# Kernel tuning notes

Hardware: AMD Instinct MI355X
Metric: run time of the kernel (lower is better)

Reference implementation:

```python
import jax, jax.numpy as jnp
import numpy as np
from jax import lax

EPS = 1e-8

def setup_inputs() -> dict:
    key = jax.random.key(0)
    ks = jax.random.split(key, 9)
    B, Cin, H, W = 16, 128, 64, 64
    C = 256
    return {
        "x":  jax.random.normal(ks[0], (B, Cin, H, W), jnp.float32),
        "w1": jax.random.normal(ks[1], (C, Cin, 3, 3), jnp.float32) * 0.02,
        "b1": jax.random.normal(ks[2], (C,), jnp.float32) * 0.02,
        "w2": jax.random.normal(ks[3], (C, C), jnp.float32) * 0.02,
        "b2": jax.random.normal(ks[4], (C,), jnp.float32) * 0.02,
        "w3": jax.random.normal(ks[5], (C, C), jnp.float32) * 0.02,
        "b3": jax.random.normal(ks[6], (C,), jnp.float32) * 0.02,
        "w4": jax.random.normal(ks[7], (C, C), jnp.float32) * 0.02,
        "b4": jax.random.normal(ks[8], (C,), jnp.float32) * 0.02,
    }

def reference(x, w1, b1, w2, b2, w3, b3, w4, b4):
    B = x.shape[0]
    # conv1: 3x3, pad 1 -> [B, 256, H, W]
    conv1 = lax.conv_general_dilated(
        x, w1, window_strides=(1, 1), padding="SAME",
        dimension_numbers=("NCHW", "OIHW", "NCHW")) + b1[None, :, None, None]
    H, W = conv1.shape[2], conv1.shape[3]
    C = conv1.shape[1]
    # gap1 -> [B, 256]; note: forward never applies relu/sigmoid (faithful)
    gap1 = conv1.mean(axis=(2, 3))
    c2 = gap1 @ w2.T + b2            # 1x1 conv on 1x1 spatial == dense
    c3 = c2 @ w3.T + b3              # [B, 256]
    # add1 = conv1 + conv1 * c3 (broadcast scale over spatial)
    add1 = conv1 * (1.0 + c3[:, :, None, None])
    gap2 = add1.mean(axis=(2, 3))    # [B, 256]
    # cosine similarity along channel dim between gap2 and add1 -> [B, H, W]
    num = jnp.einsum("bc,bchw->bhw", gap2, add1)
    n_g = jnp.maximum(jnp.linalg.norm(gap2, axis=1), EPS)[:, None, None]
    n_a = jnp.maximum(jnp.sqrt(jnp.sum(add1 * add1, axis=1)), EPS)
    cos = num / (n_g * n_a)
    r1 = cos.reshape(B, H * W)       # [B, HW]
    m1 = r1.T @ r1                   # [HW, HW] cross-batch position similarity
    # conv4: 1x1 conv -> [B, 256, H, W]
    conv4 = jnp.einsum("oc,bchw->bohw", w4, add1) + b4[None, :, None, None]
    # torch: permute to NHWC then view as [B, 256, HW] (mixes dims; faithful)
    r2 = jnp.transpose(conv4, (0, 2, 3, 1)).reshape(B, C, H * W)
    m2 = r2 @ m1                     # [B, 256, HW]
    return m2.reshape(B, C, H, W)
```

## Files before the change

kernel.cpp:

```cpp
#include <hip/hip_runtime.h>

#define EPSF 1e-8f

typedef __attribute__((ext_vector_type(8))) short bf16x8;
typedef __attribute__((ext_vector_type(16))) float f32x16;

#define MFMA32(a, b, c) __builtin_amdgcn_mfma_f32_32x32x16_bf16(a, b, c, 0, 0, 0)

__device__ __forceinline__ uint32_t splitpack(float v) {
    uint32_t u = __float_as_uint(v);
    uint32_t hb = (u + 0x7fffu + ((u >> 16) & 1u)) & 0xffff0000u;
    float rem = v - __uint_as_float(hb);
    uint32_t r = __float_as_uint(rem);
    uint32_t lb = (r + 0x7fffu + ((r >> 16) & 1u)) >> 16;
    return (hb >> 16) | (lb << 16);
}
__device__ __forceinline__ float unpackf(uint32_t p) {
    return __uint_as_float(p << 16) + __uint_as_float(p & 0xffff0000u);
}

__device__ __forceinline__ void gload_lds16(const void* src, void* dst) {
#if __has_builtin(__builtin_amdgcn_global_load_lds)
    __builtin_amdgcn_global_load_lds(
        (const __attribute__((address_space(1))) uint32_t*)src,
        (__attribute__((address_space(3))) uint32_t*)dst, 16, 0, 0);
#else
    *(uint4*)dst = *(const uint4*)src;
#endif
}

__global__ __launch_bounds__(256) void k_xpack(const float* __restrict__ x,
                                               unsigned short* __restrict__ xph,
                                               unsigned short* __restrict__ xpl) {
    const int bx = blockIdx.x;
    const int hb = bx & 15, cg = (bx >> 4) & 15, b = bx >> 8;
    const int tid = threadIdx.x;
    const int w = tid & 63, hs = tid >> 6;
    const int h = hb * 4 + hs;
    uint32_t hiw[4], low[4];
#pragma unroll
    for (int q = 0; q < 4; ++q) {
        uint32_t u0 = splitpack(x[(((b * 128 + cg * 8 + q * 2) * 64) + h) * 64 + w]);
        uint32_t u1 = splitpack(x[(((b * 128 + cg * 8 + q * 2 + 1) * 64) + h) * 64 + w]);
        hiw[q] = (u0 & 0xffffu) | (u1 << 16);
        low[q] = (u0 >> 16) | (u1 & 0xffff0000u);
    }
    const long o = ((((long)(b * 16 + cg) * 64 + h) * 64) + w) * 8;
    *(uint4*)(xph + o) = *(uint4*)hiw;
    *(uint4*)(xpl + o) = *(uint4*)low;
}

__global__ __launch_bounds__(256) void k_wpack(const float* __restrict__ w1,
                                               short* __restrict__ Bh, short* __restrict__ Bl) {
    int d = blockIdx.x * 256 + threadIdx.x;
    int j = d & 7, lane = (d >> 3) & 63, nt = (d >> 9) & 7, cp = (d >> 12) & 7, tap = d >> 15;
    int oc = nt * 32 + (lane & 31);
    int cin = cp * 16 + (lane >> 5) * 8 + j;
    uint32_t u = splitpack(w1[oc * 1152 + cin * 9 + tap]);
    Bh[d] = (short)(u & 0xffffu);
    Bl[d] = (short)(u >> 16);
}

__global__ __launch_bounds__(512, 2) void k_conv1(
        const unsigned short* __restrict__ xph, const unsigned short* __restrict__ xpl,
        const short* __restrict__ Bh, const short* __restrict__ Bl,
        const float* __restrict__ b1,
        uint32_t* __restrict__ c1p, float* __restrict__ gpart) {
    __shared__ uint4 lds[2 * 2 * 12 * 66];
    const int bxr = blockIdx.x;
    const int bx = ((bxr & 7) << 6) | (bxr >> 3);
    const int ot = bx & 1, hp = (bx >> 1) & 15, b = bx >> 5;
    const int h0 = hp * 4;
    const int tid = threadIdx.x;
    const int lane = tid & 63, wv = tid >> 6;
    const int mq = wv >> 1, nh = wv & 1;
    const int l31 = lane & 31, hbit = lane >> 5;

    f32x16 acc[2][2];
#pragma unroll
    for (int i = 0; i < 2; ++i)
#pragma unroll
        for (int j = 0; j < 2; ++j)
#pragma unroll
            for (int r = 0; r < 16; ++r) acc[i][j][r] = 0.f;

    auto stage = [&](int buf, int cp) {
#pragma unroll
        for (int i = 0; i < 3; ++i) {
            const int id = wv * 3 + i;
            const int plane = (id >= 12) ? 1 : 0;
            const int u = id - plane * 12;
            const int r6 = u >> 1, kg = u & 1;
            const int grow = h0 - 1 + r6;
            uint4* dst = &lds[((buf * 2 + plane) * 12 + u) * 66 + 1 + lane];
            if ((unsigned)grow < 64u) {
                const unsigned short* pls = plane ? xpl : xph;
                const unsigned short* src =
                    pls + ((((long)(b * 16 + cp * 2 + kg) * 64 + grow) * 64) + lane) * 8;
                gload_lds16(src, dst);
            } else {
                *dst = (uint4){0u, 0u, 0u, 0u};
            }
        }
    };

    stage(0, 0);
    if (tid < 96) {
        const int row = tid >> 1, side = tid & 1;
        lds[row * 66 + (side ? 65 : 0)] = (uint4){0u, 0u, 0u, 0u};
    }
    __syncthreads();

    bf16x8 Ahv[2][2], Alv[2][2], Bhv[3][2], Blv[3][2];
#define LOADA(tap_, par) do {                                                     \
        const int kh_ = (tap_) / 3, kw_ = (tap_) % 3;                             \
        _Pragma("unroll")                                                         \
        for (int mt = 0; mt < 2; ++mt) {                                          \
            const int rb = ((buf * 2 + 0) * 12 + (mq + kh_) * 2 + hbit) * 66      \
                           + kw_ + mt * 32 + l31;                                 \
            Ahv[par][mt] = *(const bf16x8*)&lds[rb];                              \
            Alv[par][mt] = *(const bf16x8*)&lds[rb + 12 * 66];                    \
        } } while (0)
#define LOADB(cp_, tap_, par) do {                                                \
        _Pragma("unroll")                                                         \
        for (int nt = 0; nt < 2; ++nt) {                                          \
            const int fi = (((tap_) * 8 + (cp_)) * 8 + ot * 4 + nh * 2 + nt) * 512 + lane * 8; \
            Bhv[par][nt] = *(const bf16x8*)(Bh + fi);                             \
            Blv[par][nt] = *(const bf16x8*)(Bl + fi);                             \
        } } while (0)

    LOADB(0, 0, 0);
    LOADB(0, 1, 1);
    int buf = 0;
    for (int cp = 0; cp < 8; ++cp) {
        if (cp < 7) stage(buf ^ 1, cp + 1);
        LOADA(0, 0);
#pragma unroll
        for (int tap = 0; tap < 9; ++tap) {
            if (tap < 7) {
                LOADB(cp, tap + 2, (tap + 2) % 3);
            } else if (cp < 7) {
                LOADB(cp + 1, tap - 7, (tap + 2) % 3);
            }
            if (tap < 8) LOADA(tap + 1, (tap + 1) & 1);
            const int ab = tap & 1, bb = tap % 3;
            __builtin_amdgcn_s_setprio(1);
#pragma unroll
            for (int nt = 0; nt < 2; ++nt)
#pragma unroll
                for (int mt = 0; mt < 2; ++mt) {
                    acc[mt][nt] = MFMA32(Ahv[ab][mt], Bhv[bb][nt], acc[mt][nt]);
                    acc[mt][nt] = MFMA32(Ahv[ab][mt], Blv[bb][nt], acc[mt][nt]);
                    acc[mt][nt] = MFMA32(Alv[ab][mt], Bhv[bb][nt], acc[mt][nt]);
                }
            __builtin_amdgcn_s_setprio(0);
        }
        __syncthreads();
        buf ^= 1;
    }
#undef LOADA
#undef LOADB

    const int hrow = h0 + mq;
#pragma unroll
    for (int nt = 0; nt < 2; ++nt) {
        const int oc = ot * 128 + (nh * 2 + nt) * 32 + l31;
        float g = 0.f;
#pragma unroll
        for (int mt = 0; mt < 2; ++mt)
#pragma unroll
            for (int r = 0; r < 16; ++r) g += acc[mt][nt][r];
        g += __shfl_xor(g, 32);
        if (hbit == 0) gpart[((b * 16 + hp) * 4 + mq) * 256 + oc] = g;
        const float bias = b1[oc];
#pragma unroll
        for (int mt = 0; mt < 2; ++mt) {
#pragma unroll
            for (int r = 0; r < 16; ++r) {
                const int row = (r & 3) + 8 * (r >> 2) + 4 * hbit;
                const int p = hrow * 64 + mt * 32 + row;
                c1p[((long)(b * 4096 + p)) * 256 + oc] = splitpack(acc[mt][nt][r] + bias);
            }
        }
    }
}

__global__ __launch_bounds__(256) void k_mlp(const float* __restrict__ gpart,
                                             const float* __restrict__ b1,
                                             const float* __restrict__ w2, const float* __restrict__ b2,
                                             const float* __restrict__ w3, const float* __restrict__ b3,
                                             float* __restrict__ scale, float* __restrict__ ga,
                                             float* __restrict__ n_g) {
    int b = blockIdx.x, tid = threadIdx.x;
    __shared__ float gs[256], c2s[256], red[4];
    float g = 0.f;
#pragma unroll 8
    for (int i = 0; i < 64; ++i) g += gpart[(b * 64 + i) * 256 + tid];
    gs[tid] = g * (1.f / 4096.f) + b1[tid];
    __syncthreads();
    {
        const float4* wr = (const float4*)(w2 + tid * 256);
        float a = b2[tid];
#pragma unroll 8
        for (int c4 = 0; c4 < 64; c4++) {
            float4 wv = wr[c4];
            a += wv.x * gs[c4*4] + wv.y * gs[c4*4+1] + wv.z * gs[c4*4+2] + wv.w * gs[c4*4+3];
        }
        c2s[tid] = a;
    }
    __syncthreads();
    float a3 = b3[tid];
    {
        const float4* wr = (const float4*)(w3 + tid * 256);
#pragma unroll 8
        for (int c4 = 0; c4 < 64; c4++) {
            float4 wv = wr[c4];
            a3 += wv.x * c2s[c4*4] + wv.y * c2s[c4*4+1] + wv.z * c2s[c4*4+2] + wv.w * c2s[c4*4+3];
        }
    }
    float s1 = 1.f + a3;
    float g2 = gs[tid] * s1;
    scale[b * 256 + tid] = s1;
    ga[b * 256 + tid] = g2 * s1;
    float r = g2 * g2;
    for (int off = 32; off; off >>= 1) r += __shfl_down(r, off);
    if ((tid & 63) == 0) red[tid >> 6] = r;
    __syncthreads();
    if (tid == 0) n_g[b] = fmaxf(sqrtf(red[0] + red[1] + red[2] + red[3]), EPSF);
}

__global__ __launch_bounds__(256) void k_cos(
        const uint32_t* __restrict__ c1p,
        const float* __restrict__ scale, const float* __restrict__ ga,
        const float* __restrict__ n_g, float* __restrict__ r1) {
    const int bx = blockIdx.x;
    const int pt = bx & 63, b = bx >> 6;
    const int tid = threadIdx.x;
    const int lane = tid & 63, wv = tid >> 6;
    const int half = lane >> 5, l31 = lane & 31;
    float ga8[8], sc8[8];
#pragma unroll
    for (int q = 0; q < 8; ++q) {
        ga8[q] = ga[b * 256 + l31 * 8 + q];
        sc8[q] = scale[b * 256 + l31 * 8 + q];
    }
    const float ng = n_g[b];
#pragma unroll
    for (int pp = 0; pp < 8; ++pp) {
        const int p = pt * 64 + wv * 16 + pp * 2 + half;
        const uint32_t* base = c1p + ((long)(b * 4096 + p)) * 256 + l31 * 8;
        uint4 a = *(const uint4*)base;
        uint4 bq = *(const uint4*)(base + 4);
        uint32_t pk[8] = {a.x, a.y, a.z, a.w, bq.x, bq.y, bq.z, bq.w};
        float num = 0.f, den = 0.f;
#pragma unroll
        for (int q = 0; q < 8; ++q) {
            const float v = unpackf(pk[q]);
            num += ga8[q] * v;
            const float t = sc8[q] * v;
            den += t * t;
        }
#pragma unroll
        for (int off = 1; off <= 16; off <<= 1) {
            num += __shfl_xor(num, off);
            den += __shfl_xor(den, off);
        }
        if (l31 == 0) {
            float na = fmaxf(sqrtf(den), EPSF);
            r1[b * 4096 + p] = num / (ng * na);
        }
    }
}

__global__ __launch_bounds__(256) void k_u(const float* __restrict__ r1,
                                           const float* __restrict__ w4,
                                           const float* __restrict__ b4,
                                           float* __restrict__ Uf, float* __restrict__ Dpart) {
    const int g = blockIdx.x;
    const int tid = threadIdx.x;
    __shared__ float rs[256], red[4];
    rs[tid] = r1[(g >> 4) * 4096 + (g & 15) * 256 + tid];
    __syncthreads();
    float a = 0.f;
#pragma unroll 8
    for (int o = 0; o < 256; ++o) a += rs[o] * w4[o * 256 + tid];
    Uf[(g >> 4) * 4096 + (g & 15) * 256 + tid] = a;
    float d = b4[tid] * rs[tid];
    for (int off = 32; off; off >>= 1) d += __shfl_down(d, off);
    if ((tid & 63) == 0) red[tid >> 6] = d;
    __syncthreads();
    if (tid == 0) Dpart[g] = red[0] + red[1] + red[2] + red[3];
}

__global__ __launch_bounds__(256) void k_t2(const uint32_t* __restrict__ c1p,
                                            const float* __restrict__ Uf,
                                            const float* __restrict__ scale,
                                            const float* __restrict__ Dpart,
                                            float* __restrict__ tmat) {
    __shared__ float Ac[16][256];
    __shared__ float Bc[16][260];
    __shared__ float scs[256];
    const int bx = blockIdx.x;
    const int b = bx >> 4, it = bx & 15;
    const int tid = threadIdx.x;
    const int il = tid >> 4, bp = tid & 15;
    scs[tid] = scale[b * 256 + tid];
    float acc = 0.f;
    for (int jc = 0; jc < 16; ++jc) {
        __syncthreads();
#pragma unroll
        for (int q = 0; q < 4; ++q) {
            const int f4i = tid + q * 256;
            const int row = f4i >> 6, col4 = f4i & 63;
            uint4 u = *(const uint4*)(c1p +
                ((long)(b * 4096 + it * 256 + row * 16 + jc)) * 256 + col4 * 4);
            Ac[row][col4 * 4 + 0] = unpackf(u.x) * scs[col4 * 4 + 0];
            Ac[row][col4 * 4 + 1] = unpackf(u.y) * scs[col4 * 4 + 1];
            Ac[row][col4 * 4 + 2] = unpackf(u.z) * scs[col4 * 4 + 2];
            Ac[row][col4 * 4 + 3] = unpackf(u.w) * scs[col4 * 4 + 3];
            *(float4*)&Bc[row][col4 * 4] =
                *(const float4*)(Uf + (long)row * 4096 + jc * 256 + col4 * 4);
        }
        __syncthreads();
#pragma unroll 8
        for (int j = 0; j < 256; j += 4) {
            float4 a4  = *(const float4*)&Ac[il][j];
            float4 b4v = *(const float4*)&Bc[bp][j];
            acc += a4.x * b4v.x + a4.y * b4v.y + a4.z * b4v.z + a4.w * b4v.w;
        }
    }
    float D = 0.f;
#pragma unroll
    for (int pr = 0; pr < 16; ++pr) D += Dpart[bp * 16 + pr];
    tmat[((b * 256) + it * 16 + il) * 16 + bp] = acc + D;
}

__global__ __launch_bounds__(256) void k_m2(const float* __restrict__ tmat,
                                            const float* __restrict__ r1,
                                            float* __restrict__ outb) {
    __shared__ float r1s[16][512];
    __shared__ float ts[256];
    int bx = blockIdx.x;
    int b = bx >> 7, it = (bx >> 3) & 15, pc = bx & 7;
    int tid = threadIdx.x;
    ts[tid] = tmat[(b * 256 + it * 16) * 16 + tid];
#pragma unroll
    for (int k = 0; k < 8; k++) {
        int f4i = tid + k * 256;
        int row = f4i >> 7, col = f4i & 127;
        *(float4*)&r1s[row][col * 4] = *(const float4*)(r1 + ((long)row << 12) + pc * 512 + col * 4);
    }
    __syncthreads();
    for (int il = 0; il < 16; il++) {
        float tv[16];
#pragma unroll
        for (int bp = 0; bp < 16; bp++) tv[bp] = ts[il * 16 + bp];
#pragma unroll
        for (int k = 0; k < 2; k++) {
            int p = k * 256 + tid;
            float s = 0.f;
#pragma unroll
            for (int bp = 0; bp < 16; bp++) s += tv[bp] * r1s[bp][p];
            outb[((long)b << 20) + ((long)(it * 16 + il) << 12) + pc * 512 + p] = s;
        }
    }
}

extern "C" void kernel_launch(void* const* d_in, const int* in_sizes, int n_in,
                              void* d_out, int out_size, void* d_ws, size_t ws_size,
                              hipStream_t stream) {
    const float* x  = (const float*)d_in[0];
    const float* w1 = (const float*)d_in[1];
    const float* b1 = (const float*)d_in[2];
    const float* w2 = (const float*)d_in[3];
    const float* b2 = (const float*)d_in[4];
    const float* w3 = (const float*)d_in[5];
    const float* b3 = (const float*)d_in[6];
    const float* w4 = (const float*)d_in[7];
    const float* b4 = (const float*)d_in[8];
    float* out = (float*)d_out;

    unsigned short* xph = (unsigned short*)d_out;
    unsigned short* xpl = xph + 8388608L;

    char* p = (char*)d_ws;
    uint32_t* c1p = (uint32_t*)p;  p += 16777216L * 4;
    short* Bh  = (short*)p;  p += 294912L * 2;
    short* Bl  = (short*)p;  p += 294912L * 2;
    float* gpart = (float*)p; p += 262144L * 4;
    float* scale = (float*)p; p += 4096L * 4;
    float* ga    = (float*)p; p += 4096L * 4;
    float* n_g   = (float*)p; p += 16L * 4;
    float* r1    = (float*)p; p += 65536L * 4;
    float* tmat  = (float*)p; p += 65536L * 4;
    float* Uf    = (float*)p; p += 65536L * 4;
    float* Dpart = (float*)p; p += 256L * 4;

    k_xpack <<<4096, 256, 0, stream>>>(x, xph, xpl);
    k_wpack <<<1152, 256, 0, stream>>>(w1, Bh, Bl);
    k_conv1 <<<512,  512, 0, stream>>>(xph, xpl, Bh, Bl, b1, c1p, gpart);
    k_mlp   <<<16,   256, 0, stream>>>(gpart, b1, w2, b2, w3, b3, scale, ga, n_g);
    k_cos   <<<1024, 256, 0, stream>>>(c1p, scale, ga, n_g, r1);
    k_u     <<<256,  256, 0, stream>>>(r1, w4, b4, Uf, Dpart);
    k_t2    <<<256,  256, 0, stream>>>(c1p, Uf, scale, Dpart, tmat);
    k_m2    <<<2048, 256, 0, stream>>>(tmat, r1, out);
}
```

Baseline: 223.5 us.

## Split t2 reduction four ways across blocks and deepen conv1 B-fragment prefetch

The k_t2 kernel now splits its 16-chunk reduction over the spatial dimension into four blocks per tile (1024 blocks instead of 256) and writes four partial matrices. k_m2 sums these when it loads tmat. This is meant to fill more CUs in a kernel that previously launched only 256 blocks. Separately, conv1 keeps four B-fragment register buffers instead of three and issues the B loads after the MFMAs, prefetching further ahead, which raises register pressure.

```diff
diff --git a/kernel.cpp b/kernel.cpp
--- a/kernel.cpp
+++ b/kernel.cpp
@@ -111,7 +111,7 @@
     }
     __syncthreads();
 
-    bf16x8 Ahv[2][2], Alv[2][2], Bhv[3][2], Blv[3][2];
+    bf16x8 Ahv[2][2], Alv[2][2], Bhv[4][2], Blv[4][2];
 #define LOADA(tap_, par) do {                                                     \
         const int kh_ = (tap_) / 3, kw_ = (tap_) % 3;                             \
         _Pragma("unroll")                                                         \
@@ -131,19 +131,16 @@
 
     LOADB(0, 0, 0);
     LOADB(0, 1, 1);
+    LOADB(0, 2, 2);
+    LOADB(0, 3, 3);
     int buf = 0;
     for (int cp = 0; cp < 8; ++cp) {
         if (cp < 7) stage(buf ^ 1, cp + 1);
         LOADA(0, 0);
 #pragma unroll
         for (int tap = 0; tap < 9; ++tap) {
-            if (tap < 7) {
-                LOADB(cp, tap + 2, (tap + 2) % 3);
-            } else if (cp < 7) {
-                LOADB(cp + 1, tap - 7, (tap + 2) % 3);
-            }
             if (tap < 8) LOADA(tap + 1, (tap + 1) & 1);
-            const int ab = tap & 1, bb = tap % 3;
+            const int ab = tap & 1, bb = tap & 3;
             __builtin_amdgcn_s_setprio(1);
 #pragma unroll
             for (int nt = 0; nt < 2; ++nt)
@@ -154,6 +151,15 @@
                     acc[mt][nt] = MFMA32(Alv[ab][mt], Bhv[bb][nt], acc[mt][nt]);
                 }
             __builtin_amdgcn_s_setprio(0);
+            if (tap < 5) {
+                LOADB(cp, tap + 4, tap & 3);
+            } else if (cp < 7) {
+                if (tap < 8) {
+                    LOADB(cp + 1, tap - 4, (tap - 4) & 3);
+                } else {
+                    LOADB(cp + 1, 0, 0);
+                }
+            }
         }
         __syncthreads();
         buf ^= 1;
@@ -296,17 +302,18 @@
                                             const float* __restrict__ Uf,
                                             const float* __restrict__ scale,
                                             const float* __restrict__ Dpart,
-                                            float* __restrict__ tmat) {
+                                            float* __restrict__ tmat4) {
     __shared__ float Ac[16][256];
     __shared__ float Bc[16][260];
     __shared__ float scs[256];
     const int bx = blockIdx.x;
-    const int b = bx >> 4, it = bx & 15;
+    const int kc = bx >> 8;
+    const int b = (bx >> 4) & 15, it = bx & 15;
     const int tid = threadIdx.x;
     const int il = tid >> 4, bp = tid & 15;
     scs[tid] = scale[b * 256 + tid];
     float acc = 0.f;
-    for (int jc = 0; jc < 16; ++jc) {
+    for (int jc = kc * 4; jc < kc * 4 + 4; ++jc) {
         __syncthreads();
 #pragma unroll
         for (int q = 0; q < 4; ++q) {
@@ -329,13 +336,16 @@
             acc += a4.x * b4v.x + a4.y * b4v.y + a4.z * b4v.z + a4.w * b4v.w;
         }
     }
-    float D = 0.f;
-#pragma unroll
-    for (int pr = 0; pr < 16; ++pr) D += Dpart[bp * 16 + pr];
-    tmat[((b * 256) + it * 16 + il) * 16 + bp] = acc + D;
-}
-
-__global__ __launch_bounds__(256) void k_m2(const float* __restrict__ tmat,
+    if (kc == 0) {
+        float D = 0.f;
+#pragma unroll
+        for (int pr = 0; pr < 16; ++pr) D += Dpart[bp * 16 + pr];
+        acc += D;
+    }
+    tmat4[kc * 65536 + ((b * 256) + it * 16 + il) * 16 + bp] = acc;
+}
+
+__global__ __launch_bounds__(256) void k_m2(const float* __restrict__ tmat4,
                                             const float* __restrict__ r1,
                                             float* __restrict__ outb) {
     __shared__ float r1s[16][512];
@@ -343,7 +353,10 @@
     int bx = blockIdx.x;
     int b = bx >> 7, it = (bx >> 3) & 15, pc = bx & 7;
     int tid = threadIdx.x;
-    ts[tid] = tmat[(b * 256 + it * 16) * 16 + tid];
+    {
+        const int idx = (b * 256 + it * 16) * 16 + tid;
+        ts[tid] = tmat4[idx] + tmat4[65536 + idx] + tmat4[131072 + idx] + tmat4[196608 + idx];
+    }
 #pragma unroll
     for (int k = 0; k < 8; k++) {
         int f4i = tid + k * 256;
@@ -392,7 +405,7 @@
     float* ga    = (float*)p; p += 4096L * 4;
     float* n_g   = (float*)p; p += 16L * 4;
     float* r1    = (float*)p; p += 65536L * 4;
-    float* tmat  = (float*)p; p += 65536L * 4;
+    float* tmat4 = (float*)p; p += 262144L * 4;
     float* Uf    = (float*)p; p += 65536L * 4;
     float* Dpart = (float*)p; p += 256L * 4;
 
@@ -402,6 +415,6 @@
     k_mlp   <<<16,   256, 0, stream>>>(gpart, b1, w2, b2, w3, b3, scale, ga, n_g);
     k_cos   <<<1024, 256, 0, stream>>>(c1p, scale, ga, n_g, r1);
     k_u     <<<256,  256, 0, stream>>>(r1, w4, b4, Uf, Dpart);
-    k_t2    <<<256,  256, 0, stream>>>(c1p, Uf, scale, Dpart, tmat);
-    k_m2    <<<2048, 256, 0, stream>>>(tmat, r1, out);
-}
+    k_t2    <<<1024, 256, 0, stream>>>(c1p, Uf, scale, Dpart, tmat4);
+    k_m2    <<<2048, 256, 0, stream>>>(tmat4, r1, out);
+}
```

Measured after the change: 209.9 us. 1.06x faster.
